# Kernel tuning notes

Hardware: AMD Instinct MI355X
Metric: run time of the kernel (lower is better)

The kernel has to match this reference:

```python
import jax, jax.numpy as jnp
import numpy as np

IN_FEATURES = 4096
OUT_FEATURES = 1024
BATCH = 16384
WERR = 1.0
BERR = 1.0


def setup_inputs() -> dict:
    key = jax.random.key(0)
    kx, kw = jax.random.split(key)
    X = jax.random.normal(kx, (BATCH, IN_FEATURES), dtype=jnp.float32)
    # glorot_uniform init for W, zeros for bias (as in Keras layer)
    limit = np.sqrt(6.0 / (IN_FEATURES + OUT_FEATURES)).astype(np.float32)
    W = jax.random.uniform(kw, (IN_FEATURES, OUT_FEATURES), dtype=jnp.float32,
                           minval=-limit, maxval=limit)
    bias = jnp.zeros((1, OUT_FEATURES), dtype=jnp.float32)
    return {"X": X, "W": W, "bias": bias}


def reference(X, W, bias):
    # Binarize weights/bias with sign(), scaled by Werr/Berr, then dense matmul.
    Wb = jnp.sign(W) * WERR          # [in, out], values in {-1, 0, +1}
    bb = jnp.sign(bias) * BERR       # [1, out]
    Z = jnp.matmul(X, Wb) + bb       # [batch, out]
    return Z
```

## Files before the change

### kernel.cpp

```cpp
#include <hip/hip_runtime.h>

#define M_DIM 16384
#define N_DIM 1024
#define K_DIM 4096

#define BM 256
#define BN 256
#define BK 64
#define NT (K_DIM / BK)

typedef __attribute__((ext_vector_type(4))) float f32x4;
typedef __attribute__((ext_vector_type(8))) short bf16x8;
typedef __attribute__((ext_vector_type(8))) unsigned short u16x8;

static __device__ __forceinline__ short f2bf(float f) {
  union { __bf16 h; short s; } u;
  u.h = (__bf16)f;
  return u.s;
}

static __device__ __forceinline__ void load_lds16(const void* g, void* l) {
  __builtin_amdgcn_global_load_lds(
      (const __attribute__((address_space(1))) void*)g,
      (__attribute__((address_space(3))) void*)l, 16, 0, 0);
}

__global__ __launch_bounds__(256) void wsign_transpose(
    const float* __restrict__ W, unsigned short* __restrict__ WbT) {
  __shared__ unsigned short tile[64][72];
  const int t  = (int)threadIdx.x;
  const int k0 = (int)(blockIdx.x >> 4) * 64;
  const int n0 = (int)(blockIdx.x & 15) * 64;
#pragma unroll
  for (int p = 0; p < 4; ++p) {
    const int r = p * 16 + (t >> 4);
    const int c = (t & 15) * 4;
    const float* src = W + (size_t)(k0 + r) * N_DIM + n0 + c;
#pragma unroll
    for (int j = 0; j < 4; ++j) {
      const float w = src[j];
      tile[r][c + j] = (w > 0.f) ? (unsigned short)0x3F80u
                                 : ((w < 0.f) ? (unsigned short)0xBF80u
                                              : (unsigned short)0u);
    }
  }
  __syncthreads();
  const int n  = t >> 2;
  const int kg = (t & 3) * 16;
  u16x8 o0, o1;
#pragma unroll
  for (int j = 0; j < 8; ++j) o0[j] = tile[kg + j][n];
#pragma unroll
  for (int j = 0; j < 8; ++j) o1[j] = tile[kg + 8 + j][n];
  unsigned short* dst = WbT + (size_t)(n0 + n) * K_DIM + k0 + kg;
  *(u16x8*)dst       = o0;
  *(u16x8*)(dst + 8) = o1;
}

__global__ __launch_bounds__(512, 2) void gemm_bin(
    const float* __restrict__ X, const unsigned short* __restrict__ WbT,
    const float* __restrict__ bias, float* __restrict__ Z) {
  __shared__ __align__(16) unsigned short As[2][BM * BK];
  __shared__ __align__(16) unsigned short Bs[2][BN * BK];

  const int t   = (int)threadIdx.x;
  const int l   = t & 63;
  const int wid = t >> 6;
  const int wm  = wid >> 2;
  const int wn  = wid & 3;

  const int bid = (int)blockIdx.x;
  const int swz = (bid & 7) * 32 + (bid >> 3);
  const int m0  = (swz >> 2) * BM;
  const int n0  = (swz & 3) * BN;

  const int abase = (wm * 128 + (l & 15)) * BK;
  const int bbase = (wn * 64 + (l & 15)) * BK;
  const int axk0  = (((l >> 4) + 0) ^ (l & 7)) << 3;
  const int axk1  = (((l >> 4) + 4) ^ (l & 7)) << 3;

  const float* a_src[4];
  int a_dst[4];
#pragma unroll
  for (int i = 0; i < 4; ++i) {
    const int d = i * 512 + t;
    const int row = d >> 3, g = d & 7;
    a_src[i] = X + (size_t)(m0 + row) * K_DIM + g * 8;
    a_dst[i] = row * BK + ((g ^ (row & 7)) << 3);
  }
  const unsigned short* b_src[4];
  int b_dst[4];
#pragma unroll
  for (int i = 0; i < 4; ++i) {
    const int c = i * 512 + t;
    const int n = c >> 3, gp = c & 7;
    b_src[i] = WbT + (size_t)(n0 + n) * K_DIM + (gp ^ (n & 7)) * 8;
    b_dst[i] = c * 8;
  }

  f32x4 acc[8][4] = {};
  f32x4 areg[4][2];
  bf16x8 aF[2][4], bN0[2][2], bN1[2][2];

#define SB0 __builtin_amdgcn_sched_barrier(0)
#define BAR do { SB0; __builtin_amdgcn_s_barrier(); SB0; } while (0)
#define WVM(N) do { asm volatile("s_waitcnt vmcnt(" #N ")" ::: "memory"); SB0; } while (0)
#define WLG do { asm volatile("s_waitcnt lgkmcnt(0)" ::: "memory"); SB0; } while (0)
#define PRIO1 __builtin_amdgcn_s_setprio(1)
#define PRIO0 __builtin_amdgcn_s_setprio(0)

#define ISSUE_A(KT)                                                        \
  do { SB0;                                                                \
    _Pragma("unroll") for (int i = 0; i < 4; ++i) {                        \
      areg[i][0] = *(const f32x4*)(a_src[i] + (KT));                       \
      areg[i][1] = *(const f32x4*)(a_src[i] + (KT) + 4);                   \
    } SB0;                                                                 \
  } while (0)
#define WRITE_A(BUF)                                                       \
  do {                                                                     \
    _Pragma("unroll") for (int i = 0; i < 4; ++i) {                        \
      u16x8 v;                                                             \
      _Pragma("unroll") for (int j = 0; j < 4; ++j) {                      \
        v[j]     = (unsigned short)f2bf(areg[i][0][j]);                    \
        v[4 + j] = (unsigned short)f2bf(areg[i][1][j]);                    \
      }                                                                    \
      *(u16x8*)(&As[BUF][a_dst[i]]) = v;                                   \
    }                                                                      \
  } while (0)
#define ISSUE_B(KT, BUF)                                                   \
  do { SB0;                                                                \
    _Pragma("unroll") for (int i = 0; i < 4; ++i)                          \
      load_lds16(b_src[i] + (KT), &Bs[BUF][b_dst[i]]);                     \
    SB0;                                                                   \
  } while (0)
#define READ_A(MH, AB)                                                     \
  do {                                                                     \
    _Pragma("unroll") for (int mi = 0; mi < 4; ++mi) {                     \
      aF[0][mi] = *(const bf16x8*)((AB) + abase + ((MH)*4 + mi) * 1024 + axk0); \
      aF[1][mi] = *(const bf16x8*)((AB) + abase + ((MH)*4 + mi) * 1024 + axk1); \
    }                                                                      \
  } while (0)
#define READ_B(NH, DST, BB)                                                \
  do {                                                                     \
    _Pragma("unroll") for (int ni = 0; ni < 2; ++ni) {                     \
      DST[0][ni] = *(const bf16x8*)((BB) + bbase + ((NH)*2 + ni) * 1024 + axk0); \
      DST[1][ni] = *(const bf16x8*)((BB) + bbase + ((NH)*2 + ni) * 1024 + axk1); \
    }                                                                      \
  } while (0)
#define MFMA_Q(MH, NH, BF)                                                 \
  do {                                                                     \
    _Pragma("unroll") for (int kk = 0; kk < 2; ++kk)                       \
      _Pragma("unroll") for (int mi = 0; mi < 4; ++mi)                     \
        _Pragma("unroll") for (int ni = 0; ni < 2; ++ni)                   \
          acc[(MH)*4 + mi][(NH)*2 + ni] =                                  \
              __builtin_amdgcn_mfma_f32_16x16x32_bf16(                     \
                  aF[kk][mi], BF[kk][ni], acc[(MH)*4 + mi][(NH)*2 + ni],   \
                  0, 0, 0);                                                \
  } while (0)

  ISSUE_A(0);
  ISSUE_B(0, 0);
  WVM(4);
  WRITE_A(0);
  ISSUE_A(BK);
  ISSUE_B(BK, 1);
  WVM(12);
  WLG;
  BAR;

  for (int tt = 0; tt <= NT - 3; ++tt) {
    const int buf = tt & 1;
    const unsigned short* Ab = As[buf];
    const unsigned short* Bb = Bs[buf];
    WVM(4);
    WRITE_A(buf ^ 1);
    READ_A(0, Ab);
    READ_B(0, bN0, Bb);
    BAR; WLG;
    PRIO1; MFMA_Q(0, 0, bN0); PRIO0;
    BAR;
    ISSUE_A((tt + 2) * BK);
    READ_B(1, bN1, Bb);
    BAR; WLG;
    PRIO1; MFMA_Q(0, 1, bN1); PRIO0;
    BAR;
    ISSUE_B((tt + 2) * BK, buf);
    READ_A(1, Ab);
    BAR; WLG;
    PRIO1; MFMA_Q(1, 1, bN1); PRIO0;
    BAR;
    PRIO1; MFMA_Q(1, 0, bN0); PRIO0;
    WVM(12);
    BAR;
  }

  {
    const int buf = (NT - 2) & 1;
    const unsigned short* Ab = As[buf];
    const unsigned short* Bb = Bs[buf];
    WVM(4);
    WRITE_A(buf ^ 1);
    READ_A(0, Ab);
    READ_B(0, bN0, Bb);
    BAR; WLG;
    PRIO1; MFMA_Q(0, 0, bN0); PRIO0;
    BAR;
    READ_B(1, bN1, Bb);
    BAR; WLG;
    PRIO1; MFMA_Q(0, 1, bN1); PRIO0;
    BAR;
    READ_A(1, Ab);
    BAR; WLG;
    PRIO1; MFMA_Q(1, 1, bN1); PRIO0;
    BAR;
    PRIO1; MFMA_Q(1, 0, bN0); PRIO0;
    WVM(0);
    BAR;
  }
  {
    const int buf = (NT - 1) & 1;
    const unsigned short* Ab = As[buf];
    const unsigned short* Bb = Bs[buf];
    READ_A(0, Ab);
    READ_B(0, bN0, Bb);
    READ_B(1, bN1, Bb);
    MFMA_Q(0, 0, bN0);
    MFMA_Q(0, 1, bN1);
    READ_A(1, Ab);
    MFMA_Q(1, 1, bN1);
    MFMA_Q(1, 0, bN0);
  }

#pragma unroll
  for (int ni = 0; ni < 4; ++ni) {
    const int col = n0 + wn * 64 + ni * 16 + (l & 15);
    const float b  = bias[col];
    const float bs = (b > 0.f) ? 1.f : ((b < 0.f) ? -1.f : 0.f);
#pragma unroll
    for (int mi = 0; mi < 8; ++mi) {
      const int row = m0 + wm * 128 + mi * 16 + ((l >> 4) << 2);
#pragma unroll
      for (int j = 0; j < 4; ++j)
        Z[(size_t)(row + j) * N_DIM + col] = acc[mi][ni][j] + bs;
    }
  }
#undef SB0
#undef BAR
#undef WVM
#undef WLG
#undef PRIO1
#undef PRIO0
#undef ISSUE_A
#undef WRITE_A
#undef ISSUE_B
#undef READ_A
#undef READ_B
#undef MFMA_Q
}

__global__ __launch_bounds__(256) void naive_fb(
    const float* __restrict__ X, const float* __restrict__ W,
    const float* __restrict__ bias, float* __restrict__ Z) {
  const size_t id = (size_t)blockIdx.x * 256 + threadIdx.x;
  const int m = (int)(id >> 10), n = (int)(id & 1023);
  float acc = 0.f;
  for (int k = 0; k < K_DIM; ++k) {
    const float w = W[(size_t)k * N_DIM + n];
    const float s = (w > 0.f) ? 1.f : ((w < 0.f) ? -1.f : 0.f);
    acc += X[(size_t)m * K_DIM + k] * s;
  }
  const float b = bias[n];
  Z[id] = acc + ((b > 0.f) ? 1.f : ((b < 0.f) ? -1.f : 0.f));
}

extern "C" void kernel_launch(void* const* d_in, const int* in_sizes, int n_in,
                              void* d_out, int out_size, void* d_ws, size_t ws_size,
                              hipStream_t stream) {
  const float* X    = (const float*)d_in[0];
  const float* W    = (const float*)d_in[1];
  const float* bias = (const float*)d_in[2];
  float* Z = (float*)d_out;

  const size_t need = (size_t)N_DIM * K_DIM * sizeof(unsigned short);
  if (ws_size >= need) {
    unsigned short* WbT = (unsigned short*)d_ws;
    wsign_transpose<<<dim3((K_DIM / 64) * (N_DIM / 64)), dim3(256), 0, stream>>>(W, WbT);
    gemm_bin<<<dim3((M_DIM / BM) * (N_DIM / BN)), dim3(512), 0, stream>>>(X, WbT, bias, Z);
  } else {
    naive_fb<<<dim3((size_t)M_DIM * N_DIM / 256), dim3(256), 0, stream>>>(X, W, bias, Z);
  }
}
```

Measured before the change: 188.4 us.

## Split A prefetch into halves and prefetch next-tile LDS fragments across iterations

Splits the global-to-register loads and bf16 conversion of X into two half-tiles, staggered across the four MFMA phases of each k-step. It double-buffers the A and B fragment registers so the first quadrant's fragments for the next k-tile are read from LDS during the current tile. Partial lgkmcnt waits replace the full waits. The aim is to hide LDS and global latency behind MFMA work, at the cost of more live vector registers and more fragile barrier and wait counting. Some leftover unused macro variants are defined and then undefined.

```diff
diff --git a/kernel.cpp b/kernel.cpp
--- a/kernel.cpp
+++ b/kernel.cpp
@@ -79,15 +79,13 @@
   const int axk0  = (((l >> 4) + 0) ^ (l & 7)) << 3;
   const int axk1  = (((l >> 4) + 4) ^ (l & 7)) << 3;
 
-  const float* a_src[4];
-  int a_dst[4];
-#pragma unroll
-  for (int i = 0; i < 4; ++i) {
-    const int d = i * 512 + t;
-    const int row = d >> 3, g = d & 7;
-    a_src[i] = X + (size_t)(m0 + row) * K_DIM + g * 8;
-    a_dst[i] = row * BK + ((g ^ (row & 7)) << 3);
-  }
+  const int rA = t >> 3, g = t & 7;
+  const float* sA0 = X + (size_t)(m0 + rA) * K_DIM + g * 8;
+  const float* sA1 = X + (size_t)(m0 + 64 + rA) * K_DIM + g * 8;
+  const float* sB0 = X + (size_t)(m0 + 128 + rA) * K_DIM + g * 8;
+  const float* sB1 = X + (size_t)(m0 + 192 + rA) * K_DIM + g * 8;
+  const int adst = rA * BK + ((g ^ (rA & 7)) << 3);
+
   const unsigned short* b_src[4];
   int b_dst[4];
 #pragma unroll
@@ -99,32 +97,40 @@
   }
 
   f32x4 acc[8][4] = {};
-  f32x4 areg[4][2];
-  bf16x8 aF[2][4], bN0[2][2], bN1[2][2];
+  f32x4 arA[2][2], arB[2][2];
+  bf16x8 aF0[2][4], aF1[2][4];
+  bf16x8 bR0[2][2], bR1[2][2];
 
 #define SB0 __builtin_amdgcn_sched_barrier(0)
 #define BAR do { SB0; __builtin_amdgcn_s_barrier(); SB0; } while (0)
 #define WVM(N) do { asm volatile("s_waitcnt vmcnt(" #N ")" ::: "memory"); SB0; } while (0)
-#define WLG do { asm volatile("s_waitcnt lgkmcnt(0)" ::: "memory"); SB0; } while (0)
+#define WLGC(N) do { asm volatile("s_waitcnt lgkmcnt(" #N ")" ::: "memory"); SB0; } while (0)
 #define PRIO1 __builtin_amdgcn_s_setprio(1)
 #define PRIO0 __builtin_amdgcn_s_setprio(0)
 
-#define ISSUE_A(KT)                                                        \
+#define IA_H1(KT)                                                          \
   do { SB0;                                                                \
-    _Pragma("unroll") for (int i = 0; i < 4; ++i) {                        \
-      areg[i][0] = *(const f32x4*)(a_src[i] + (KT));                       \
-      areg[i][1] = *(const f32x4*)(a_src[i] + (KT) + 4);                   \
-    } SB0;                                                                 \
-  } while (0)
-#define WRITE_A(BUF)                                                       \
-  do {                                                                     \
-    _Pragma("unroll") for (int i = 0; i < 4; ++i) {                        \
+    arA[0][0] = *(const f32x4*)(sA0 + (KT));                               \
+    arA[0][1] = *(const f32x4*)(sA0 + (KT) + 4);                           \
+    arA[1][0] = *(const f32x4*)(sA1 + (KT));                               \
+    arA[1][1] = *(const f32x4*)(sA1 + (KT) + 4); SB0;                      \
+  } while (0)
+#define IA_H2(KT)                                                          \
+  do { SB0;                                                                \
+    arB[0][0] = *(const f32x4*)(sB0 + (KT));                               \
+    arB[0][1] = *(const f32x4*)(sB0 + (KT) + 4);                           \
+    arB[1][0] = *(const f32x4*)(sB1 + (KT));                               \
+    arB[1][1] = *(const f32x4*)(sB1 + (KT) + 4); SB0;                      \
+  } while (0)
+#define WR_H(BUF, AR, OFS)                                                 \
+  do {                                                                     \
+    _Pragma("unroll") for (int i = 0; i < 2; ++i) {                        \
       u16x8 v;                                                             \
       _Pragma("unroll") for (int j = 0; j < 4; ++j) {                      \
-        v[j]     = (unsigned short)f2bf(areg[i][0][j]);                    \
-        v[4 + j] = (unsigned short)f2bf(areg[i][1][j]);                    \
+        v[j]     = (unsigned short)f2bf(AR[i][0][j]);                      \
+        v[4 + j] = (unsigned short)f2bf(AR[i][1][j]);                      \
       }                                                                    \
-      *(u16x8*)(&As[BUF][a_dst[i]]) = v;                                   \
+      *(u16x8*)(&As[BUF][adst + (OFS) + i * 4096]) = v;                    \
     }                                                                      \
   } while (0)
 #define ISSUE_B(KT, BUF)                                                   \
@@ -133,65 +139,153 @@
       load_lds16(b_src[i] + (KT), &Bs[BUF][b_dst[i]]);                     \
     SB0;                                                                   \
   } while (0)
-#define READ_A(MH, AB)                                                     \
+#define READ_AF(DST, MH, AB)                                               \
   do {                                                                     \
     _Pragma("unroll") for (int mi = 0; mi < 4; ++mi) {                     \
-      aF[0][mi] = *(const bf16x8*)((AB) + abase + ((MH)*4 + mi) * 1024 + axk0); \
-      aF[1][mi] = *(const bf16x8*)((AB) + abase + ((MH)*4 + mi) * 1024 + axk1); \
+      DST[0][mi] = *(const bf16x8*)((AB) + abase + ((MH)*4 + mi) * 1024 + axk0); \
+      DST[1][mi] = *(const bf16x8*)((AB) + abase + ((MH)*4 + mi) * 1024 + axk1); \
     }                                                                      \
   } while (0)
-#define READ_B(NH, DST, BB)                                                \
+#define READ_BF(DST, NH, BB)                                               \
   do {                                                                     \
     _Pragma("unroll") for (int ni = 0; ni < 2; ++ni) {                     \
       DST[0][ni] = *(const bf16x8*)((BB) + bbase + ((NH)*2 + ni) * 1024 + axk0); \
       DST[1][ni] = *(const bf16x8*)((BB) + bbase + ((NH)*2 + ni) * 1024 + axk1); \
     }                                                                      \
   } while (0)
-#define MFMA_Q(MH, NH, BF)                                                 \
-  do {                                                                     \
+#define MFMA_Q(MH, NH, AFR, BFR)                                           \
+  do { PRIO1;                                                              \
     _Pragma("unroll") for (int kk = 0; kk < 2; ++kk)                       \
       _Pragma("unroll") for (int mi = 0; mi < 4; ++mi)                     \
         _Pragma("unroll") for (int ni = 0; ni < 2; ++ni)                   \
           acc[(MH)*4 + mi][(NH)*2 + ni] =                                  \
               __builtin_amdgcn_mfma_f32_16x16x32_bf16(                     \
-                  aF[kk][mi], BF[kk][ni], acc[(MH)*4 + mi][(NH)*2 + ni],   \
+                  AFR[kk][mi], BFR[kk][ni], acc[(MH)*4 + mi][(NH)*2 + ni], \
                   0, 0, 0);                                                \
-  } while (0)
-
-  ISSUE_A(0);
+    PRIO0;                                                                 \
+  } while (0)
+
+#define STEADY(TT, NA, NB)                                                 \
+  do {                                                                     \
+    const int buf = (TT) & 1;                                              \
+    const unsigned short* Ab = As[buf];                                    \
+    const unsigned short* Bb = Bs[buf];                                    \
+                                                                  \
+    WVM(4);                                 \
+    WR_H(buf ^ 1, arA, 0);                                                 \
+    IA_H1(((TT) + 1) * BK);            \
+    READ_BF(NB, 1, Bb);                                                    \
+    BAR; WLGC(6);                   \
+    MFMA_Q(0, 0, aF0, NA);                                                 \
+    BAR;                                                                   \
+                                                                  \
+    READ_AF(aF1, 1, Ab);                                                   \
+    IA_H2(((TT) + 2) * BK);                        \
+    BAR; WLGC(8);                            \
+    MFMA_Q(0, 1, aF0, NB);                                                 \
+    BAR;                                                                   \
+                                                                  \
+    WVM(4);                             \
+    WR_H(buf ^ 1, arB, 8192);                                              \
+    ISSUE_B(((TT) + 2) * BK, buf);                                         \
+    BAR; WLGC(0);                          \
+    MFMA_Q(1, 1, aF1, NB);                                                 \
+    BAR;                                                                   \
+                                                                  \
+    READ_AF(aF0, 0, As[buf ^ 1]);                                          \
+    READ_BF(NA, 0, Bs[buf ^ 1]);      \
+    BAR;                                  \
+    MFMA_Q(1, 0, aF1, NA##_hold);                                          \
+    BAR;                                                                   \
+  } while (0)
+
+#undef STEADY
+#define STEADY2(TT, NAcur, NAnext)                                         \
+  do {                                                                     \
+    const int buf = (TT) & 1;                                              \
+    const unsigned short* Ab = As[buf];                                    \
+    const unsigned short* Bb = Bs[buf];                                    \
+             \
+    WVM(4);                                                                \
+    WR_H(buf ^ 1, arA, 0);                                                 \
+    IA_H2(((TT) + 1) * BK);                       \
+    READ_BF(NAnext, 1, Bb);                         \
+    BAR; WLGC(6);                                                          \
+    MFMA_Q(0, 0, aF0, NAcur);                                              \
+    BAR;                                                                   \
+                                                                  \
+    READ_AF(aF1, 1, Ab);                                                   \
+    IA_H1(((TT) + 2) * BK);                       \
+    BAR; WLGC(8);                                                          \
+    MFMA_Q(0, 1, aF0, NAnext);                                             \
+    BAR;                                                                   \
+                                                                  \
+    WVM(4);                                  \
+    WR_H(buf ^ 1, arB, 8192);                                              \
+    ISSUE_B(((TT) + 2) * BK, buf);                                         \
+    BAR; WLGC(0);                                                          \
+    MFMA_Q(1, 1, aF1, NAnext);                                             \
+    BAR;                                                                   \
+               \
+    READ_AF(aF0, 0, As[buf ^ 1]);                                          \
+    READ_BF(NAcur, 0, Bs[buf ^ 1]);                                        \
+    BAR;                                                                   \
+    MFMA_Q(1, 0, aF1, NAcur);                \
+    BAR;                                                                   \
+  } while (0)
+#undef STEADY2
+#define STEADY3(TT, NAcur, NBcur)                                          \
+  do {                                                                     \
+    const int buf = (TT) & 1;                                              \
+    const unsigned short* Ab = As[buf];                                    \
+    const unsigned short* Bb = Bs[buf];                                    \
+             \
+    WVM(4);                                                                \
+    WR_H(buf ^ 1, arA, 0);                                                 \
+    IA_H2(((TT) + 1) * BK);                                                \
+    READ_BF(NBcur, 1, Bb);                                                 \
+    BAR; WLGC(6);                                                          \
+    MFMA_Q(0, 0, aF0, NAcur);                                              \
+    BAR;                                                                   \
+                                                                  \
+    READ_AF(aF1, 1, Ab);                                                   \
+    IA_H1(((TT) + 2) * BK);                                                \
+    BAR; WLGC(8);                                                          \
+    MFMA_Q(0, 1, aF0, NBcur);                                              \
+    BAR;                                                                   \
+                                                                  \
+    WVM(4);                                                                \
+    WR_H(buf ^ 1, arB, 8192);                                              \
+    ISSUE_B(((TT) + 2) * BK, buf);                                         \
+    BAR; WLGC(0);                                                          \
+    MFMA_Q(1, 1, aF1, NBcur);                         \
+    BAR;                                                                   \
+                       \
+    READ_AF(aF0, 0, As[buf ^ 1]);                                          \
+    READ_BF(NBcur, 0, Bs[buf ^ 1]);                                        \
+    BAR;                                                                   \
+    MFMA_Q(1, 0, aF1, NAcur);                   \
+    BAR;                                                                   \
+  } while (0)
+
+  IA_H1(0); IA_H2(0);
   ISSUE_B(0, 0);
+  WVM(8);
+  WR_H(0, arA, 0);
   WVM(4);
-  WRITE_A(0);
-  ISSUE_A(BK);
+  WR_H(0, arB, 8192);
+  IA_H1(BK);
   ISSUE_B(BK, 1);
-  WVM(12);
-  WLG;
+  WVM(8);
+  WLGC(0);
   BAR;
-
-  for (int tt = 0; tt <= NT - 3; ++tt) {
-    const int buf = tt & 1;
-    const unsigned short* Ab = As[buf];
-    const unsigned short* Bb = Bs[buf];
-    WVM(4);
-    WRITE_A(buf ^ 1);
-    READ_A(0, Ab);
-    READ_B(0, bN0, Bb);
-    BAR; WLG;
-    PRIO1; MFMA_Q(0, 0, bN0); PRIO0;
-    BAR;
-    ISSUE_A((tt + 2) * BK);
-    READ_B(1, bN1, Bb);
-    BAR; WLG;
-    PRIO1; MFMA_Q(0, 1, bN1); PRIO0;
-    BAR;
-    ISSUE_B((tt + 2) * BK, buf);
-    READ_A(1, Ab);
-    BAR; WLG;
-    PRIO1; MFMA_Q(1, 1, bN1); PRIO0;
-    BAR;
-    PRIO1; MFMA_Q(1, 0, bN0); PRIO0;
-    WVM(12);
-    BAR;
+  READ_AF(aF0, 0, As[0]);
+  READ_BF(bR0, 0, Bs[0]);
+
+  for (int tp = 0; tp < (NT - 2) / 2; ++tp) {
+    const int tt = 2 * tp;
+    STEADY3(tt, bR0, bR1);
+    STEADY3(tt + 1, bR1, bR0);
   }
 
   {
@@ -199,36 +293,39 @@
     const unsigned short* Ab = As[buf];
     const unsigned short* Bb = Bs[buf];
     WVM(4);
-    WRITE_A(buf ^ 1);
-    READ_A(0, Ab);
-    READ_B(0, bN0, Bb);
-    BAR; WLG;
-    PRIO1; MFMA_Q(0, 0, bN0); PRIO0;
-    BAR;
-    READ_B(1, bN1, Bb);
-    BAR; WLG;
-    PRIO1; MFMA_Q(0, 1, bN1); PRIO0;
-    BAR;
-    READ_A(1, Ab);
-    BAR; WLG;
-    PRIO1; MFMA_Q(1, 1, bN1); PRIO0;
-    BAR;
-    PRIO1; MFMA_Q(1, 0, bN0); PRIO0;
+    WR_H(buf ^ 1, arA, 0);
+    IA_H2((NT - 1) * BK);
+    READ_BF(bR1, 1, Bb);
+    BAR; WLGC(6);
+    MFMA_Q(0, 0, aF0, bR0);
+    BAR;
+    READ_AF(aF1, 1, Ab);
+    BAR; WLGC(8);
+    MFMA_Q(0, 1, aF0, bR1);
+    BAR;
     WVM(0);
+    WR_H(buf ^ 1, arB, 8192);
+    BAR; WLGC(0);
+    MFMA_Q(1, 1, aF1, bR1);
+    BAR;
+    READ_AF(aF0, 0, As[buf ^ 1]);
+    READ_BF(bR1, 0, Bs[buf ^ 1]);
+    BAR;
+    MFMA_Q(1, 0, aF1, bR0);
     BAR;
   }
   {
     const int buf = (NT - 1) & 1;
     const unsigned short* Ab = As[buf];
     const unsigned short* Bb = Bs[buf];
-    READ_A(0, Ab);
-    READ_B(0, bN0, Bb);
-    READ_B(1, bN1, Bb);
-    MFMA_Q(0, 0, bN0);
-    MFMA_Q(0, 1, bN1);
-    READ_A(1, Ab);
-    MFMA_Q(1, 1, bN1);
-    MFMA_Q(1, 0, bN0);
+    WLGC(0);
+    MFMA_Q(0, 0, aF0, bR1);
+    READ_BF(bR0, 1, Bb);
+    READ_AF(aF1, 1, Ab);
+    WLGC(0);
+    MFMA_Q(0, 1, aF0, bR0);
+    MFMA_Q(1, 1, aF1, bR0);
+    MFMA_Q(1, 0, aF1, bR1);
   }
 
 #pragma unroll
@@ -244,18 +341,6 @@
         Z[(size_t)(row + j) * N_DIM + col] = acc[mi][ni][j] + bs;
     }
   }
-#undef SB0
-#undef BAR
-#undef WVM
-#undef WLG
-#undef PRIO1
-#undef PRIO0
-#undef ISSUE_A
-#undef WRITE_A
-#undef ISSUE_B
-#undef READ_A
-#undef READ_B
-#undef MFMA_Q
 }
 
 __global__ __launch_bounds__(256) void naive_fb(
```

Measured after the change: 577.8 us. 3.07x slower.
